# Kernel optimization log

Hardware: AMD Instinct MI355X
Metric: run time of the kernel (lower is better)

## Reference

```python
import jax, jax.numpy as jnp
import numpy as np


def setup_inputs() -> dict:
    key = jax.random.key(0)
    ks = jax.random.split(key, 5)
    b, l, ns, ni, d = 128, 64, 32, 16, 256
    scale = 1.0 / np.sqrt(d)
    return {
        "token_features": jax.random.normal(ks[0], (b, l, d), jnp.float32),
        "w_route_ws": jax.random.normal(ks[1], (l, ns, d), jnp.float32) * scale,
        "w_pose_ws": jax.random.normal(ks[2], (l, ns, d, d), jnp.float32) * scale,
        "w_route_si": jax.random.normal(ks[3], (ns, ni, d), jnp.float32) * scale,
        "w_pose_si": jax.random.normal(ks[4], (ns, ni, d, d), jnp.float32) * scale,
    }


def reference(token_features, w_route_ws, w_pose_ws, w_route_si, w_pose_si):
    d_model = token_features.shape[-1]

    # ---- route words -> slots ----
    # token activations ('norm' strategy): mean over d_model -> (b, l)
    a_words = jnp.sum(token_features, axis=-1) / d_model
    # routing logits (b, l, n_slot_caps), softmax over slot caps
    c_ws = jax.nn.softmax(jnp.einsum('lnj,blj->bln', w_route_ws, token_features), axis=-1)
    weighted_c = jnp.einsum('bls,bl->bs', c_ws, a_words)            # (b, ns)
    a_slots = weighted_c / jnp.sum(a_words, axis=-1, keepdims=True)  # (b, ns)
    # pose votes (b, l, ns, d) then weighted aggregation + divisive normalization
    u_hat_slots = jnp.einsum('lnij,blj->blni', w_pose_ws, token_features)
    u_slots = jnp.einsum('bls,bl,blsk->bsk', c_ws, a_words, u_hat_slots) / weighted_c[:, :, None]

    # ---- route slots -> intents ----
    c_si = jax.nn.softmax(jnp.einsum('sij,bsj->bsi', w_route_si, u_slots), axis=-1)
    weighted_c2 = jnp.einsum('bsi,bs->bi', c_si, a_slots)            # (b, ni)
    a_intents = weighted_c2 / jnp.sum(a_slots, axis=-1, keepdims=True)
    u_hat_intents = jnp.einsum('sijk,bsk->bsik', w_pose_si, u_slots)  # (b, ns, ni, d)
    u_intents = jnp.einsum('bsi,bs,bsik->bik', c_si, a_slots, u_hat_intents) / weighted_c2[:, :, None]

    return a_slots, u_slots, a_intents, u_intents
```

## Files before the change

### kernel.cpp

```cpp
#include <hip/hip_runtime.h>
#include <math.h>

#define B  128
#define L  64
#define NS 32
#define NI 16
#define D  256

typedef __attribute__((ext_vector_type(8))) short bf16x8;
typedef __attribute__((ext_vector_type(4))) float f32x4;

__device__ __forceinline__ float wave_reduce_sum(float v) {
#pragma unroll
  for (int off = 32; off; off >>= 1) v += __shfl_xor(v, off, 64);
  return v;
}
__device__ __forceinline__ float wave_reduce_max(float v) {
#pragma unroll
  for (int off = 32; off; off >>= 1) v = fmaxf(v, __shfl_xor(v, off, 64));
  return v;
}

__device__ __forceinline__ uint cvt_pk_bf16(float a, float b) {
  uint r;
  asm("v_cvt_pk_bf16_f32 %0, %1, %2" : "=v"(r) : "v"(a), "v"(b));
  return r;
}
__device__ __forceinline__ void split4(float4 v, uint2& h, uint2& lo) {
  h.x = cvt_pk_bf16(v.x, v.y);
  h.y = cvt_pk_bf16(v.z, v.w);
  float h0 = __uint_as_float(h.x << 16);
  float h1 = __uint_as_float(h.x & 0xFFFF0000u);
  float h2 = __uint_as_float(h.y << 16);
  float h3 = __uint_as_float(h.y & 0xFFFF0000u);
  lo.x = cvt_pk_bf16(v.x - h0, v.y - h1);
  lo.y = cvt_pk_bf16(v.z - h2, v.w - h3);
}

__device__ __forceinline__ void dma16(const void* g, void* l) {
  __builtin_amdgcn_global_load_lds(
      (const __attribute__((address_space(1))) void*)g,
      (__attribute__((address_space(3))) void*)l, 16, 0, 0);
}

__device__ __forceinline__ int swzA(int row, int kcol) {
  int byte = (row << 7) + (kcol << 1);
  byte ^= (row & 7) << 4;
  return byte >> 1;
}

__global__ __launch_bounds__(256) void kx_split(
    const float* __restrict__ tf, ushort* __restrict__ xh,
    ushort* __restrict__ xl) {
  int tile = blockIdx.x;
  int l  = tile >> 2;
  int jc = (tile & 3) * 64;
  int t  = threadIdx.x;
  int row = t >> 1;
  int k0  = (t & 1) * 32;
  const float* src = tf + ((size_t)row * L + l) * D + jc + k0;
  ushort* ht = xh + (size_t)tile * 8192;
  ushort* lt = xl + (size_t)tile * 8192;
#pragma unroll
  for (int c = 0; c < 8; ++c) {
    float4 v = *(const float4*)(src + c * 4);
    uint2 h, lo;
    split4(v, h, lo);
    int ix = swzA(row, k0 + c * 4);
    *(uint2*)&ht[ix] = h;
    *(uint2*)&lt[ix] = lo;
  }
}

__global__ __launch_bounds__(256) void k1_route_words(
    const float* __restrict__ tf, const float* __restrict__ wr,
    float* __restrict__ wlsT, float* __restrict__ a_words) {
  int bl = blockIdx.x;
  int b  = bl >> 6;
  int l  = bl & (L - 1);
  int t  = threadIdx.x;
  int wave = t >> 6, lane = t & 63;
  __shared__ float sx[D];
  __shared__ float slog[NS];
  __shared__ float s_aw;
  sx[t] = tf[bl * D + t];
  __syncthreads();
  const float* wbase = wr + l * NS * D;
#pragma unroll
  for (int r = 0; r < 8; ++r) {
    int n = wave * 8 + r;
    const float* w = wbase + n * D;
    float p = 0.f;
#pragma unroll
    for (int jj = 0; jj < 4; ++jj) {
      int j = lane + jj * 64;
      p = fmaf(w[j], sx[j], p);
    }
    p = wave_reduce_sum(p);
    if (lane == 0) slog[n] = p;
  }
  if (wave == 0) {
    float p = sx[lane] + sx[lane + 64] + sx[lane + 128] + sx[lane + 192];
    p = wave_reduce_sum(p);
    if (lane == 0) s_aw = p * (1.f / D);
  }
  __syncthreads();
  if (wave == 0) {
    float aw = s_aw;
    float v = (lane < NS) ? slog[lane] : -INFINITY;
    float m = wave_reduce_max(v);
    float e = (lane < NS) ? __expf(v - m) : 0.f;
    float s = wave_reduce_sum(e);
    if (lane < NS) wlsT[(l * NS + lane) * B + b] = (e / s) * aw;
    if (lane == 0) a_words[bl] = aw;
  }
}

__global__ __launch_bounds__(64) void k2_slots_agg(
    const float* __restrict__ wlsT, const float* __restrict__ a_words,
    float* __restrict__ weighted_c, float* __restrict__ a_slots) {
  int b = blockIdx.x;
  int lane = threadIdx.x;
  float aw = a_words[b * L + lane];
  float sa = wave_reduce_sum(aw);
  if (lane < NS) {
    float wc = 0.f;
    for (int l = 0; l < L; ++l) wc += wlsT[(l * NS + lane) * B + b];
    weighted_c[b * NS + lane] = wc;
    a_slots[b * NS + lane] = wc / sa;
  }
}

__global__ __launch_bounds__(256, 2) void k3_mfma(
    const ushort* __restrict__ xh, const ushort* __restrict__ xl,
    const float* __restrict__ wp, const float* __restrict__ wlsT,
    float* __restrict__ part, int nsplit) {
  __shared__ ushort Ah[2][4096], Al[2][4096];
  __shared__ float  Wt[2][4096];
  __shared__ float  swl[4096];

  int bx    = blockIdx.x;
  int xcd   = bx & 7;
  int bh    = (bx >> 3) & 1;
  int chunk = bx >> 4;
  int pidx  = chunk * 8 + xcd;
  int sp = pidx % nsplit;
  int rr = pidx / nsplit;
  int it = rr & 3, s = rr >> 2;
  int i0 = it * 64;
  int lchunk = L / nsplit, l0 = sp * lchunk;
  int steps  = lchunk * 4;

  int t = threadIdx.x, lane = t & 63, wv = t >> 6;
  int fr = lane & 15, q = lane >> 4;

  int wofs[4];
#pragma unroll
  for (int wi = 0; wi < 4; ++wi) {
    int row  = (wv * 4 + wi) * 4 + (lane >> 4);
    int soff = ((lane & 15) * 16) ^ ((row & 7) << 4);
    wofs[wi] = row * 1024 + soff;
  }
  int aofs = wv * 1024 + lane * 8;

  for (int of = t; of < lchunk * 64; of += 256) {
    int li = of >> 6, b = of & 63;
    swl[of] = wlsT[((size_t)(l0 + li) * NS + s) * B + bh * 64 + b];
  }
  asm volatile("s_waitcnt vmcnt(0) lgkmcnt(0)" ::: "memory");
  __builtin_amdgcn_s_barrier();

  f32x4 P[4], R[4];
#pragma unroll
  for (int mi = 0; mi < 4; ++mi) { P[mi] = (f32x4)0.f; R[mi] = (f32x4)0.f; }

  auto issue = [&](int step) {
    int cs = step < steps ? step : steps - 1;
    int pb = step & 1;
    int l = l0 + (cs >> 2), jci = cs & 3;
    size_t tile = ((size_t)l * 4 + jci) * 8192 + (size_t)bh * 4096;
    const ushort* th = xh + tile;
    const ushort* tl = xl + tile;
    dma16(th + aofs,       &Ah[pb][wv * 1024]);
    dma16(th + aofs + 512, &Ah[pb][wv * 1024 + 512]);
    dma16(tl + aofs,       &Al[pb][wv * 1024]);
    dma16(tl + aofs + 512, &Al[pb][wv * 1024 + 512]);
    const char* wbase = (const char*)(wp + ((size_t)l * NS + s) * (D * D) +
                                      (size_t)i0 * D + jci * 64);
#pragma unroll
    for (int wi = 0; wi < 4; ++wi)
      dma16(wbase + wofs[wi], (char*)&Wt[pb][0] + (wv * 4 + wi) * 1024);
  };

  issue(0);
  for (int step = 0; step < steps; ++step) {
    issue(step + 1);
    asm volatile("s_waitcnt vmcnt(8)" ::: "memory");
    __builtin_amdgcn_s_barrier();
    int pb = step & 1;
    int wrow = wv * 16 + fr;
    int wkey = (wrow & 7) << 4;
    const char* wb = (const char*)&Wt[pb][0];
    bf16x8 fh[2], fl[2];
#pragma unroll
    for (int k2 = 0; k2 < 2; ++k2) {
      int base = wrow * 256 + k2 * 128 + q * 32;
      float4 w0 = *(const float4*)(wb + ((base) ^ wkey));
      float4 w1 = *(const float4*)(wb + ((base + 16) ^ wkey));
      uint2 h0, e0, h1, e1;
      split4(w0, h0, e0);
      split4(w1, h1, e1);
      uint4 hu = {h0.x, h0.y, h1.x, h1.y};
      uint4 lu = {e0.x, e0.y, e1.x, e1.y};
      fh[k2] = __builtin_bit_cast(bf16x8, hu);
      fl[k2] = __builtin_bit_cast(bf16x8, lu);
    }
#pragma unroll
    for (int k2 = 0; k2 < 2; ++k2) {
#pragma unroll
      for (int mi = 0; mi < 4; ++mi) {
        int arow  = mi * 16 + fr;
        int abyte = (arow * 128 + (k2 * 32 + q * 8) * 2) ^ ((arow & 7) << 4);
        bf16x8 ah = *(const bf16x8*)((const char*)&Ah[pb][0] + abyte);
        bf16x8 al = *(const bf16x8*)((const char*)&Al[pb][0] + abyte);
        P[mi] = __builtin_amdgcn_mfma_f32_16x16x32_bf16(ah, fh[k2], P[mi], 0, 0, 0);
        P[mi] = __builtin_amdgcn_mfma_f32_16x16x32_bf16(ah, fl[k2], P[mi], 0, 0, 0);
        P[mi] = __builtin_amdgcn_mfma_f32_16x16x32_bf16(al, fh[k2], P[mi], 0, 0, 0);
      }
    }
    if ((step & 3) == 3) {
      int sl = step >> 2;
#pragma unroll
      for (int mi = 0; mi < 4; ++mi) {
        f32x4 s4 = *(const f32x4*)&swl[sl * 64 + mi * 16 + q * 4];
        R[mi] += s4 * P[mi];
        P[mi] = (f32x4)0.f;
      }
    }
    asm volatile("s_waitcnt lgkmcnt(0)" ::: "memory");
    __builtin_amdgcn_s_barrier();
  }

  float* pout = part + ((size_t)sp * NS + s) * (B * D);
  int col = i0 + wv * 16 + fr;
#pragma unroll
  for (int mi = 0; mi < 4; ++mi)
#pragma unroll
    for (int e = 0; e < 4; ++e) {
      int bb = bh * 64 + mi * 16 + q * 4 + e;
      pout[(size_t)bb * D + col] = R[mi][e];
    }
}

__global__ __launch_bounds__(256) void k3r_reduce(
    const float* __restrict__ part, const float* __restrict__ wc,
    float* __restrict__ u_slots, int nsplit) {
  int idx = blockIdx.x * 256 + threadIdx.x;
  int i  = idx & (D - 1);
  int sb = idx >> 8;
  int b  = sb & (B - 1);
  int s  = sb >> 7;
  float v = 0.f;
  for (int sp = 0; sp < nsplit; ++sp)
    v += part[(size_t)sp * (NS * B * D) + idx];
  u_slots[((size_t)b * NS + s) * D + i] = v / wc[b * NS + s];
}

__global__ __launch_bounds__(64) void k4_route_si(
    const float* __restrict__ u_slots, const float* __restrict__ wr_si,
    const float* __restrict__ a_slots, float* __restrict__ w2) {
  int bs = blockIdx.x;
  int s  = bs & (NS - 1);
  int lane = threadIdx.x;
  __shared__ float su[D];
  __shared__ float slog[NI];
#pragma unroll
  for (int jj = 0; jj < 4; ++jj) su[lane + jj * 64] = u_slots[bs * D + lane + jj * 64];
  __syncthreads();
  for (int i = 0; i < NI; ++i) {
    const float* w = wr_si + (s * NI + i) * D;
    float p = 0.f;
#pragma unroll
    for (int jj = 0; jj < 4; ++jj) {
      int j = lane + jj * 64;
      p = fmaf(w[j], su[j], p);
    }
    p = wave_reduce_sum(p);
    if (lane == 0) slog[i] = p;
  }
  __syncthreads();
  float v = (lane < NI) ? slog[lane] : -INFINITY;
  float m = wave_reduce_max(v);
  float e = (lane < NI) ? __expf(v - m) : 0.f;
  float ssum = wave_reduce_sum(e);
  if (lane < NI) w2[bs * NI + lane] = (e / ssum) * a_slots[bs];
}

__global__ __launch_bounds__(64) void k5_intents_agg(
    const float* __restrict__ w2, const float* __restrict__ a_slots,
    float* __restrict__ wc2, float* __restrict__ a_intents) {
  int b = blockIdx.x;
  int lane = threadIdx.x;
  float as = (lane < NS) ? a_slots[b * NS + lane] : 0.f;
  float sas = wave_reduce_sum(as);
  if (lane < NI) {
    float wc = 0.f;
    for (int s = 0; s < NS; ++s) wc += w2[(b * NS + s) * NI + lane];
    wc2[b * NI + lane] = wc;
    a_intents[b * NI + lane] = wc / sas;
  }
}

__global__ __launch_bounds__(256) void k6_wsum(
    const float* __restrict__ wps, float* __restrict__ wsum) {
  __shared__ float red[4][D];
  int si = blockIdx.x;
  int t  = threadIdx.x;
  int k4 = (t & 63) * 4;
  int jg = t >> 6;
  const float* base = wps + (size_t)si * D * D;
  float4 acc = {0.f, 0.f, 0.f, 0.f};
  for (int j = jg; j < D; j += 4) {
    float4 v = *(const float4*)(base + (size_t)j * D + k4);
    acc.x += v.x; acc.y += v.y; acc.z += v.z; acc.w += v.w;
  }
  *(float4*)&red[jg][k4] = acc;
  __syncthreads();
  wsum[si * D + t] = (red[0][t] + red[1][t]) + (red[2][t] + red[3][t]);
}

__global__ __launch_bounds__(256) void k7_uintents(
    const float* __restrict__ u_slots, const float* __restrict__ w2,
    const float* __restrict__ wsum, const float* __restrict__ wc2,
    float* __restrict__ u_intents) {
  int bi = blockIdx.x;
  int b = bi >> 4, i = bi & (NI - 1);
  int k = threadIdx.x;
  float acc = 0.f;
  for (int s = 0; s < NS; ++s) {
    float w = w2[(b * NS + s) * NI + i];
    acc = fmaf(w * u_slots[(b * NS + s) * D + k], wsum[(s * NI + i) * D + k], acc);
  }
  u_intents[bi * D + k] = acc / wc2[bi];
}

extern "C" void kernel_launch(void* const* d_in, const int* in_sizes, int n_in,
                              void* d_out, int out_size, void* d_ws, size_t ws_size,
                              hipStream_t stream) {
  const float* tf    = (const float*)d_in[0];
  const float* wr_ws = (const float*)d_in[1];
  const float* wp_ws = (const float*)d_in[2];
  const float* wr_si = (const float*)d_in[3];
  const float* wp_si = (const float*)d_in[4];

  float* out       = (float*)d_out;
  float* a_slots   = out;
  float* u_slots   = a_slots + B * NS;
  float* a_intents = u_slots + B * NS * D;
  float* u_intents = a_intents + B * NI;

  float* ws         = (float*)d_ws;
  float* wlsT       = ws;
  float* a_words    = wlsT + L * NS * B;
  float* weighted_c = a_words + B * L;
  float* w2         = weighted_c + B * NS;
  float* wc2        = w2 + B * NS * NI;
  float* wsum       = wc2 + B * NI;
  ushort* xh        = (ushort*)(wsum + NS * NI * D);
  ushort* xl        = xh + (size_t)L * 4 * 8192;
  float*  part      = (float*)(xl + (size_t)L * 4 * 8192);

  const size_t base_f  = 473088 + 2097152;
  const size_t chunk_f = (size_t)NS * B * D;
  size_t avail_f = ws_size / sizeof(float);
  int nsplit = 1;
  if (avail_f >= base_f + 4 * chunk_f)      nsplit = 4;
  else if (avail_f >= base_f + 2 * chunk_f) nsplit = 2;

  kx_split<<<L * 4, 256, 0, stream>>>(tf, xh, xl);
  k1_route_words<<<B * L, 256, 0, stream>>>(tf, wr_ws, wlsT, a_words);
  k2_slots_agg<<<B, 64, 0, stream>>>(wlsT, a_words, weighted_c, a_slots);
  k3_mfma<<<NS * 4 * 2 * nsplit, 256, 0, stream>>>(xh, xl, wp_ws, wlsT, part, nsplit);
  k3r_reduce<<<(NS * B * D) / 256, 256, 0, stream>>>(part, weighted_c, u_slots, nsplit);
  k6_wsum<<<NS * NI, 256, 0, stream>>>(wp_si, wsum);
  k4_route_si<<<B * NS, 64, 0, stream>>>(u_slots, wr_si, a_slots, w2);
  k5_intents_agg<<<B, 64, 0, stream>>>(w2, a_slots, wc2, a_intents);
  k7_uintents<<<B * NI, 256, 0, stream>>>(u_slots, w2, wsum, wc2, u_intents);
}
```

Before: 296.9 us.

## Retile pose-vote MFMA kernel to full-batch 128x128 tiles with streamed routing weights

The main MFMA kernel now covers all 128 batch rows and 128 output columns per block, using a K-step of 32 instead of 64. This removes the batch-half split, so each W_pose tile is loaded once rather than twice. Routing weights are streamed per layer through a small double-buffered LDS slice instead of being preloaded. The token split layout is reorganised into 32-wide K tiles with a new swizzle, and nsplit can go up to 8. In exchange, accumulator registers double, the block count drops, and the larger split produces more partial-sum traffic for the reduction kernel.

```diff
diff --git a/kernel.cpp b/kernel.cpp
--- a/kernel.cpp
+++ b/kernel.cpp
@@ -43,32 +43,29 @@
       (__attribute__((address_space(3))) void*)l, 16, 0, 0);
 }
 
-__device__ __forceinline__ int swzA(int row, int kcol) {
-  int byte = (row << 7) + (kcol << 1);
-  byte ^= (row & 7) << 4;
-  return byte >> 1;
-}
-
 __global__ __launch_bounds__(256) void kx_split(
     const float* __restrict__ tf, ushort* __restrict__ xh,
     ushort* __restrict__ xl) {
-  int tile = blockIdx.x;
-  int l  = tile >> 2;
-  int jc = (tile & 3) * 64;
+  int bx = blockIdx.x;
+  int l  = bx >> 2, jp = bx & 3;
   int t  = threadIdx.x;
-  int row = t >> 1;
-  int k0  = (t & 1) * 32;
-  const float* src = tf + ((size_t)row * L + l) * D + jc + k0;
-  ushort* ht = xh + (size_t)tile * 8192;
-  ushort* lt = xl + (size_t)tile * 8192;
-#pragma unroll
-  for (int c = 0; c < 8; ++c) {
-    float4 v = *(const float4*)(src + c * 4);
-    uint2 h, lo;
-    split4(v, h, lo);
-    int ix = swzA(row, k0 + c * 4);
-    *(uint2*)&ht[ix] = h;
-    *(uint2*)&lt[ix] = lo;
+  int row = t >> 1, sub = t & 1;
+  int tile = bx * 2 + sub;
+  const float* src = tf + ((size_t)row * L + l) * D + jp * 64 + sub * 32;
+  ushort* ht = xh + (size_t)tile * 4096 + row * 32;
+  ushort* lt = xl + (size_t)tile * 4096 + row * 32;
+#pragma unroll
+  for (int u = 0; u < 4; ++u) {
+    float4 v0 = *(const float4*)(src + u * 8);
+    float4 v1 = *(const float4*)(src + u * 8 + 4);
+    uint2 h0, e0, h1, e1;
+    split4(v0, h0, e0);
+    split4(v1, h1, e1);
+    int up = (u ^ (row & 3)) * 8;
+    uint4 hu = {h0.x, h0.y, h1.x, h1.y};
+    uint4 lu = {e0.x, e0.y, e1.x, e1.y};
+    *(uint4*)&ht[up] = hu;
+    *(uint4*)&lt[up] = lu;
   }
 }
 
@@ -137,104 +134,97 @@
     float* __restrict__ part, int nsplit) {
   __shared__ ushort Ah[2][4096], Al[2][4096];
   __shared__ float  Wt[2][4096];
-  __shared__ float  swl[4096];
-
-  int bx    = blockIdx.x;
-  int xcd   = bx & 7;
-  int bh    = (bx >> 3) & 1;
-  int chunk = bx >> 4;
-  int pidx  = chunk * 8 + xcd;
-  int sp = pidx % nsplit;
-  int rr = pidx / nsplit;
-  int it = rr & 3, s = rr >> 2;
-  int i0 = it * 64;
+  __shared__ float  swl[2][256];
+
+  int bx  = blockIdx.x;
+  int sp  = bx & (nsplit - 1);
+  int rem = bx / nsplit;
+  int ih  = rem & 1, s = rem >> 1;
+  int i0  = ih * 128;
   int lchunk = L / nsplit, l0 = sp * lchunk;
-  int steps  = lchunk * 4;
+  int steps  = lchunk * 8;
 
   int t = threadIdx.x, lane = t & 63, wv = t >> 6;
   int fr = lane & 15, q = lane >> 4;
-
-  int wofs[4];
-#pragma unroll
-  for (int wi = 0; wi < 4; ++wi) {
-    int row  = (wv * 4 + wi) * 4 + (lane >> 4);
-    int soff = ((lane & 15) * 16) ^ ((row & 7) << 4);
-    wofs[wi] = row * 1024 + soff;
-  }
-  int aofs = wv * 1024 + lane * 8;
-
-  for (int of = t; of < lchunk * 64; of += 256) {
-    int li = of >> 6, b = of & 63;
-    swl[of] = wlsT[((size_t)(l0 + li) * NS + s) * B + bh * 64 + b];
-  }
-  asm volatile("s_waitcnt vmcnt(0) lgkmcnt(0)" ::: "memory");
-  __builtin_amdgcn_s_barrier();
-
-  f32x4 P[4], R[4];
-#pragma unroll
-  for (int mi = 0; mi < 4; ++mi) { P[mi] = (f32x4)0.f; R[mi] = (f32x4)0.f; }
-
-  auto issue = [&](int step) {
-    int cs = step < steps ? step : steps - 1;
-    int pb = step & 1;
-    int l = l0 + (cs >> 2), jci = cs & 3;
-    size_t tile = ((size_t)l * 4 + jci) * 8192 + (size_t)bh * 4096;
-    const ushort* th = xh + tile;
-    const ushort* tl = xl + tile;
-    dma16(th + aofs,       &Ah[pb][wv * 1024]);
-    dma16(th + aofs + 512, &Ah[pb][wv * 1024 + 512]);
-    dma16(tl + aofs,       &Al[pb][wv * 1024]);
-    dma16(tl + aofs + 512, &Al[pb][wv * 1024 + 512]);
-    const char* wbase = (const char*)(wp + ((size_t)l * NS + s) * (D * D) +
-                                      (size_t)i0 * D + jci * 64);
-#pragma unroll
-    for (int wi = 0; wi < 4; ++wi)
-      dma16(wbase + wofs[wi], (char*)&Wt[pb][0] + (wv * 4 + wi) * 1024);
+  int wrow8 = lane >> 3;
+  int wu    = lane & 7;
+  int wswz  = ((wu ^ wrow8) << 4);
+
+  f32x4 P[8][2], R[8][2];
+#pragma unroll
+  for (int mi = 0; mi < 8; ++mi)
+#pragma unroll
+    for (int ni = 0; ni < 2; ++ni) { P[mi][ni] = (f32x4)0.f; R[mi][ni] = (f32x4)0.f; }
+
+  auto issue = [&](int tn) {
+    int cs = tn < steps ? tn : steps - 1;
+    int pb = tn & 1;
+    int li = cs >> 3, jci = cs & 7;
+    int l  = l0 + li;
+    const ushort* th = xh + ((size_t)l * 8 + jci) * 4096;
+    const ushort* tl = xl + ((size_t)l * 8 + jci) * 4096;
+    dma16(th + wv * 1024 + lane * 8,       &Ah[pb][wv * 1024]);
+    dma16(th + wv * 1024 + 512 + lane * 8, &Ah[pb][wv * 1024 + 512]);
+    dma16(tl + wv * 1024 + lane * 8,       &Al[pb][wv * 1024]);
+    dma16(tl + wv * 1024 + 512 + lane * 8, &Al[pb][wv * 1024 + 512]);
+    const char* wb = (const char*)wp +
+                     (((size_t)l * NS + s) * (D * D) + (size_t)i0 * D) * 4 +
+                     jci * 128;
+#pragma unroll
+    for (int wi = 0; wi < 4; ++wi) {
+      int rbase = wv * 32 + wi * 8;
+      dma16(wb + (size_t)(rbase + wrow8) * 1024 + wswz,
+            (char*)&Wt[pb][0] + rbase * 128);
+    }
+    const char* sws = (const char*)(wlsT + ((size_t)l * NS + s) * B);
+    dma16(sws + lane * 16, &swl[(cs >> 3) & 1][0]);
   };
 
   issue(0);
-  for (int step = 0; step < steps; ++step) {
-    issue(step + 1);
-    asm volatile("s_waitcnt vmcnt(8)" ::: "memory");
+  for (int tt = 0; tt < steps; ++tt) {
+    issue(tt + 1);
+    asm volatile("s_waitcnt vmcnt(9)" ::: "memory");
     __builtin_amdgcn_s_barrier();
-    int pb = step & 1;
-    int wrow = wv * 16 + fr;
-    int wkey = (wrow & 7) << 4;
-    const char* wb = (const char*)&Wt[pb][0];
+    int pb = tt & 1;
     bf16x8 fh[2], fl[2];
 #pragma unroll
-    for (int k2 = 0; k2 < 2; ++k2) {
-      int base = wrow * 256 + k2 * 128 + q * 32;
-      float4 w0 = *(const float4*)(wb + ((base) ^ wkey));
-      float4 w1 = *(const float4*)(wb + ((base + 16) ^ wkey));
+    for (int ni = 0; ni < 2; ++ni) {
+      int wr = wv * 32 + ni * 16 + fr;
+      const char* wbp = (const char*)&Wt[pb][0] + wr * 128;
+      int key = fr & 7;
+      float4 w0 = *(const float4*)(wbp + (((q * 2 + 0) ^ key) << 4));
+      float4 w1 = *(const float4*)(wbp + (((q * 2 + 1) ^ key) << 4));
       uint2 h0, e0, h1, e1;
       split4(w0, h0, e0);
       split4(w1, h1, e1);
       uint4 hu = {h0.x, h0.y, h1.x, h1.y};
       uint4 lu = {e0.x, e0.y, e1.x, e1.y};
-      fh[k2] = __builtin_bit_cast(bf16x8, hu);
-      fl[k2] = __builtin_bit_cast(bf16x8, lu);
-    }
-#pragma unroll
-    for (int k2 = 0; k2 < 2; ++k2) {
-#pragma unroll
-      for (int mi = 0; mi < 4; ++mi) {
-        int arow  = mi * 16 + fr;
-        int abyte = (arow * 128 + (k2 * 32 + q * 8) * 2) ^ ((arow & 7) << 4);
-        bf16x8 ah = *(const bf16x8*)((const char*)&Ah[pb][0] + abyte);
-        bf16x8 al = *(const bf16x8*)((const char*)&Al[pb][0] + abyte);
-        P[mi] = __builtin_amdgcn_mfma_f32_16x16x32_bf16(ah, fh[k2], P[mi], 0, 0, 0);
-        P[mi] = __builtin_amdgcn_mfma_f32_16x16x32_bf16(ah, fl[k2], P[mi], 0, 0, 0);
-        P[mi] = __builtin_amdgcn_mfma_f32_16x16x32_bf16(al, fh[k2], P[mi], 0, 0, 0);
+      fh[ni] = __builtin_bit_cast(bf16x8, hu);
+      fl[ni] = __builtin_bit_cast(bf16x8, lu);
+    }
+#pragma unroll
+    for (int mi = 0; mi < 8; ++mi) {
+      int ar = mi * 16 + fr;
+      int au = ar * 32 + ((q ^ (fr & 3)) << 3);
+      bf16x8 ah = *(const bf16x8*)&Ah[pb][au];
+      bf16x8 al = *(const bf16x8*)&Al[pb][au];
+#pragma unroll
+      for (int ni = 0; ni < 2; ++ni) {
+        P[mi][ni] = __builtin_amdgcn_mfma_f32_16x16x32_bf16(ah, fh[ni], P[mi][ni], 0, 0, 0);
+        P[mi][ni] = __builtin_amdgcn_mfma_f32_16x16x32_bf16(ah, fl[ni], P[mi][ni], 0, 0, 0);
+        P[mi][ni] = __builtin_amdgcn_mfma_f32_16x16x32_bf16(al, fh[ni], P[mi][ni], 0, 0, 0);
       }
     }
-    if ((step & 3) == 3) {
-      int sl = step >> 2;
-#pragma unroll
-      for (int mi = 0; mi < 4; ++mi) {
-        f32x4 s4 = *(const f32x4*)&swl[sl * 64 + mi * 16 + q * 4];
-        R[mi] += s4 * P[mi];
-        P[mi] = (f32x4)0.f;
+    if ((tt & 7) == 7) {
+      int lb = (tt >> 3) & 1;
+#pragma unroll
+      for (int mi = 0; mi < 8; ++mi) {
+        f32x4 s4 = *(const f32x4*)&swl[lb][mi * 16 + q * 4];
+#pragma unroll
+        for (int ni = 0; ni < 2; ++ni) {
+          R[mi][ni] += s4 * P[mi][ni];
+          P[mi][ni] = (f32x4)0.f;
+        }
       }
     }
     asm volatile("s_waitcnt lgkmcnt(0)" ::: "memory");
@@ -242,13 +232,16 @@
   }
 
   float* pout = part + ((size_t)sp * NS + s) * (B * D);
-  int col = i0 + wv * 16 + fr;
-#pragma unroll
-  for (int mi = 0; mi < 4; ++mi)
-#pragma unroll
-    for (int e = 0; e < 4; ++e) {
-      int bb = bh * 64 + mi * 16 + q * 4 + e;
-      pout[(size_t)bb * D + col] = R[mi][e];
+#pragma unroll
+  for (int mi = 0; mi < 8; ++mi)
+#pragma unroll
+    for (int ni = 0; ni < 2; ++ni) {
+      int col = i0 + wv * 32 + ni * 16 + fr;
+#pragma unroll
+      for (int e = 0; e < 4; ++e) {
+        int bb = mi * 16 + q * 4 + e;
+        pout[(size_t)bb * D + col] = R[mi][ni][e];
+      }
     }
 }
 
@@ -367,20 +360,21 @@
   float* wc2        = w2 + B * NS * NI;
   float* wsum       = wc2 + B * NI;
   ushort* xh        = (ushort*)(wsum + NS * NI * D);
-  ushort* xl        = xh + (size_t)L * 4 * 8192;
-  float*  part      = (float*)(xl + (size_t)L * 4 * 8192);
+  ushort* xl        = xh + (size_t)L * 8 * 4096;
+  float*  part      = (float*)(xl + (size_t)L * 8 * 4096);
 
   const size_t base_f  = 473088 + 2097152;
   const size_t chunk_f = (size_t)NS * B * D;
   size_t avail_f = ws_size / sizeof(float);
   int nsplit = 1;
-  if (avail_f >= base_f + 4 * chunk_f)      nsplit = 4;
+  if (avail_f >= base_f + 8 * chunk_f)      nsplit = 8;
+  else if (avail_f >= base_f + 4 * chunk_f) nsplit = 4;
   else if (avail_f >= base_f + 2 * chunk_f) nsplit = 2;
 
   kx_split<<<L * 4, 256, 0, stream>>>(tf, xh, xl);
   k1_route_words<<<B * L, 256, 0, stream>>>(tf, wr_ws, wlsT, a_words);
   k2_slots_agg<<<B, 64, 0, stream>>>(wlsT, a_words, weighted_c, a_slots);
-  k3_mfma<<<NS * 4 * 2 * nsplit, 256, 0, stream>>>(xh, xl, wp_ws, wlsT, part, nsplit);
+  k3_mfma<<<NS * 2 * nsplit, 256, 0, stream>>>(xh, xl, wp_ws, wlsT, part, nsplit);
   k3r_reduce<<<(NS * B * D) / 256, 256, 0, stream>>>(part, weighted_c, u_slots, nsplit);
   k6_wsum<<<NS * NI, 256, 0, stream>>>(wp_si, wsum);
   k4_route_si<<<B * NS, 64, 0, stream>>>(u_slots, wr_si, a_slots, w2);
```

Result: faster. 244.4 us (-17.7%).
